# Performance work log

Hardware: AMD Instinct MI355X
Metric: run time of the kernel (lower is better)

## Reference

```python
import jax, jax.numpy as jnp
import numpy as np

B, S, H = 2, 1024, 2048
HQ, HKV, D = 16, 4, 128
E, K, CAP = 32, 4, 512
IM, SIM = 512, 1024
EPS = 1e-6
THETA = 1.0e6
T = B * S


def setup_inputs() -> dict:
    key = jax.random.key(0)
    ks = jax.random.split(key, 16)
    r = lambda i, shape, s=0.02: jax.random.normal(ks[i], shape, dtype=jnp.float32) * s
    return {
        "hidden_states": jax.random.normal(ks[0], (T, H), dtype=jnp.float32),
        "positions": jnp.tile(jnp.arange(S, dtype=jnp.int32), B),
        "ln1_w": jnp.ones((H,), jnp.float32),
        "ln2_w": jnp.ones((H,), jnp.float32),
        "wq": r(1, (H, HQ * D)),
        "wk": r(2, (H, HKV * D)),
        "wv": r(3, (H, HKV * D)),
        "wo": r(4, (HQ * D, H)),
        "qn_w": jnp.ones((D,), jnp.float32),
        "kn_w": jnp.ones((D,), jnp.float32),
        "gate_w": r(5, (H, E), 0.05),
        "expert_bias": r(6, (E,), 0.1),
        "w_gate_e": r(7, (E, H, IM)),
        "w_up_e": r(8, (E, H, IM)),
        "w_down_e": r(9, (E, IM, H)),
        "ws_gate": r(10, (H, SIM)),
        "ws_up": r(11, (H, SIM)),
        "ws_down": r(12, (SIM, H)),
    }


def _rms(x, w):
    return x * jax.lax.rsqrt(jnp.mean(x * x, axis=-1, keepdims=True) + EPS) * w


def _forward(hidden_states, positions, ln1_w, ln2_w, wq, wk, wv, wo, qn_w, kn_w,
             gate_w, expert_bias, w_gate_e, w_up_e, w_down_e, ws_gate, ws_up, ws_down):
    # --- attention block ---
    resid = hidden_states
    h = _rms(hidden_states, ln1_w)
    q = (h @ wq).reshape(T, HQ, D)
    k = (h @ wk).reshape(T, HKV, D)
    v = (h @ wv).reshape(T, HKV, D)
    q = _rms(q, qn_w)  # per-head qk-norm
    k = _rms(k, kn_w)
    # neox-style RoPE over full head_dim
    inv = 1.0 / (THETA ** (jnp.arange(0, D, 2, dtype=jnp.float32) / D))
    fr = positions.astype(jnp.float32)[:, None] * inv  # [T, D/2]
    cos, sin = jnp.cos(fr)[:, None, :], jnp.sin(fr)[:, None, :]
    def rope(x):
        x1, x2 = jnp.split(x, 2, axis=-1)
        return jnp.concatenate([x1 * cos - x2 * sin, x2 * cos + x1 * sin], axis=-1)
    q, k = rope(q), rope(k)
    qb = q.reshape(B, S, HQ, D)
    kb = jnp.repeat(k.reshape(B, S, HKV, D), HQ // HKV, axis=2)  # GQA expand
    vb = jnp.repeat(v.reshape(B, S, HKV, D), HQ // HKV, axis=2)
    sc = jnp.einsum('bqhd,bkhd->bhqk', qb, kb) * (D ** -0.5)
    causal = jnp.tril(jnp.ones((S, S), dtype=bool))
    sc = jnp.where(causal, sc, jnp.float32(-1e30))
    p = jax.nn.softmax(sc, axis=-1)
    ao = jnp.einsum('bhqk,bkhd->bqhd', p, vb).reshape(T, HQ * D)
    h = ao @ wo + resid
    resid = h
    h = _rms(h, ln2_w)
    # --- shared experts (dense MLP) ---
    shared = (jax.nn.silu(h @ ws_gate) * (h @ ws_up)) @ ws_down
    # --- sigmoid router with correction bias (bias only for selection) ---
    scores = jax.nn.sigmoid(h @ gate_w)          # [T, E]
    _, idx = jax.lax.top_k(scores + expert_bias, K)
    w = jnp.take_along_axis(scores, idx, axis=-1)
    w = w / jnp.sum(w, axis=-1, keepdims=True)   # renormalize top-k probs
    # --- capacity-based dispatch / grouped GEMM / combine ---
    flat_e = idx.reshape(-1)                     # [T*K]
    flat_t = jnp.repeat(jnp.arange(T), K)
    flat_w = w.reshape(-1)
    order = jnp.argsort(flat_e)                  # stable sort by expert
    se, st, sw = flat_e[order], flat_t[order], flat_w[order]
    counts = jnp.bincount(flat_e, length=E)
    starts = jnp.concatenate([jnp.zeros((1,), counts.dtype), jnp.cumsum(counts)[:-1]])
    pos = jnp.arange(T * K) - starts[se]         # slot within expert
    valid = pos < CAP                            # capacity guard (never trips in practice)
    posc = jnp.minimum(pos, CAP - 1)
    xbuf = jnp.zeros((E, CAP, H), h.dtype).at[se, posc].add(
        jnp.where(valid[:, None], h[st], 0.0))   # [E, CAP, H]
    inter = jax.nn.silu(jnp.einsum('ech,ehi->eci', xbuf, w_gate_e)) \
            * jnp.einsum('ech,ehi->eci', xbuf, w_up_e)
    obuf = jnp.einsum('eci,eih->ech', inter, w_down_e)
    y = obuf[se, posc] * jnp.where(valid, sw, 0.0)[:, None]
    moe = jnp.zeros((T, H), h.dtype).at[st].add(y)
    return resid + moe + shared


def reference(hidden_states, positions, ln1_w, ln2_w, wq, wk, wv, wo, qn_w, kn_w,
              gate_w, expert_bias, w_gate_e, w_up_e, w_down_e, ws_gate, ws_up, ws_down):
    return _forward(hidden_states, positions, ln1_w, ln2_w, wq, wk, wv, wo, qn_w, kn_w,
                    gate_w, expert_bias, w_gate_e, w_up_e, w_down_e, ws_gate, ws_up, ws_down)
```

## Files before the change

### kernel.cpp

```cpp
#include <hip/hip_runtime.h>
#include <stdint.h>

typedef unsigned short u16;
typedef unsigned short bf16u;
typedef unsigned int u32;
typedef _Float16 f16;
typedef __attribute__((ext_vector_type(8))) short bf16x8;
typedef __attribute__((ext_vector_type(8))) _Float16 f16x8;
typedef __attribute__((ext_vector_type(4))) float f32x4;

#define T_N 2048
#define H_N 2048
#define S_N 1024
#define B_N 2
#define HQ_N 16
#define HKV_N 4
#define D_N 128
#define E_N 32
#define K_TOP 4
#define CAP_N 512
#define IM_N 512
#define SIM_N 1024
#define QD_N 2048
#define KD_N 512
#define QKV_N 3072
#define NFLAT (T_N*K_TOP)
#define RGRP 128
#define NGRP (NFLAT/RGRP)

#define SC_H1   1024.0f
#define SC_W    512.0f
#define SC_QK   2048.0f
#define SC_P    4096.0f
#define SC_V    2048.0f
#define OSC_QKV (1.0f/524288.0f)
#define OSC_OPJ (1.0f/1048576.0f)

__device__ __forceinline__ float bf2f(bf16u x){ return __uint_as_float(((u32)x)<<16); }
__device__ __forceinline__ bf16u f2bf(float f){
  u32 u = __float_as_uint(f);
  u32 r = (u + 0x7FFFu + ((u>>16)&1u)) >> 16;
  return (bf16u)r;
}
__device__ __forceinline__ u32 pkbf(float a, float b){
  u32 ua = __float_as_uint(a), ub = __float_as_uint(b);
  u32 ra = (ua + 0x7FFFu + ((ua>>16)&1u)) >> 16;
  u32 rb = (ub + 0x7FFFu + ((ub>>16)&1u)) & 0xFFFF0000u;
  return ra | rb;
}
__device__ __forceinline__ void split2h(float x, u16& h, u16& l){
  f16 hh = (f16)x;
  f16 ll = (f16)(x - (float)hh);
  h = __builtin_bit_cast(u16, hh);
  l = __builtin_bit_cast(u16, ll);
}
__device__ __forceinline__ f32x4 mfma16b(bf16x8 a, bf16x8 b, f32x4 c){
  return __builtin_amdgcn_mfma_f32_16x16x32_bf16(a,b,c,0,0,0);
}
__device__ __forceinline__ f32x4 mfma16h(f16x8 a, f16x8 b, f32x4 c){
  return __builtin_amdgcn_mfma_f32_16x16x32_f16(a,b,c,0,0,0);
}
__device__ __forceinline__ void gl_lds16(const void* g, void* l){
  __builtin_amdgcn_global_load_lds((const __attribute__((address_space(1))) u32*)g,
                                   (__attribute__((address_space(3))) u32*)l, 16, 0, 0);
}

__global__ __launch_bounds__(256) void transpose_f32(const float* __restrict__ in,
                                                     float* __restrict__ out, int R, int C){
  __shared__ float tile[32][33];
  int rb = blockIdx.x*32, cb = blockIdx.y*32;
  int tx = threadIdx.x, ty = threadIdx.y;
  #pragma unroll
  for (int kk=0;kk<4;kk++)
    tile[ty+kk*8][tx] = in[(size_t)(rb+ty+kk*8)*C + cb + tx];
  __syncthreads();
  #pragma unroll
  for (int kk=0;kk<4;kk++)
    out[(size_t)(cb+ty+kk*8)*R + rb + tx] = tile[tx][ty+kk*8];
}

__global__ __launch_bounds__(256) void transpose_cvt_g(const float* __restrict__ in,
                                                       bf16u* __restrict__ out, int R, int C){
  __shared__ float tile[64*64];
  size_t zo = (size_t)blockIdx.z * R * C;
  int rb = blockIdx.x*64, cb = blockIdx.y*64;
  int tid = threadIdx.x, wave = tid>>6, lane = tid&63;
  #pragma unroll
  for (int p=0;p<4;p++){
    int r = p*16 + wave*4 + (lane>>4);
    const float* src = in + zo + (size_t)(rb + r)*C + cb + (lane&15)*4;
    gl_lds16(src, &tile[(p*16 + wave*4)*64]);
  }
  __syncthreads();
  int c = tid>>2, rq = (tid&3)*16;
  u16 tmp[16];
  #pragma unroll
  for (int j=0;j<16;j++) tmp[j] = f2bf(tile[(rq+j)*64 + c]);
  uint4 w0, w1;
  w0.x=(u32)tmp[0]|((u32)tmp[1]<<16);  w0.y=(u32)tmp[2]|((u32)tmp[3]<<16);
  w0.z=(u32)tmp[4]|((u32)tmp[5]<<16);  w0.w=(u32)tmp[6]|((u32)tmp[7]<<16);
  w1.x=(u32)tmp[8]|((u32)tmp[9]<<16);  w1.y=(u32)tmp[10]|((u32)tmp[11]<<16);
  w1.z=(u32)tmp[12]|((u32)tmp[13]<<16); w1.w=(u32)tmp[14]|((u32)tmp[15]<<16);
  bf16u* dst = out + zo + (size_t)(cb+c)*R + rb + rq;
  *(uint4*)dst = w0;
  *(uint4*)(dst+8) = w1;
}

__global__ __launch_bounds__(256) void transpose_cvt_split16(const float* __restrict__ in,
                                                             u16* __restrict__ oh,
                                                             u16* __restrict__ ol,
                                                             int R, int C, float scale){
  __shared__ u16 th[32][33];
  __shared__ u16 tl[32][33];
  int rb = blockIdx.x*32, cb = blockIdx.y*32;
  int tx = threadIdx.x, ty = threadIdx.y;
  #pragma unroll
  for (int kk=0;kk<4;kk++){
    float x = in[(size_t)(rb+ty+kk*8)*C + cb + tx] * scale;
    u16 hh, ll; split2h(x, hh, ll);
    th[ty+kk*8][tx] = hh; tl[ty+kk*8][tx] = ll;
  }
  __syncthreads();
  #pragma unroll
  for (int kk=0;kk<4;kk++){
    size_t idx = (size_t)(cb+ty+kk*8)*R + rb + tx;
    oh[idx] = th[tx][ty+kk*8];
    ol[idx] = tl[tx][ty+kk*8];
  }
}

__global__ __launch_bounds__(256) void rmsnorm_bf16(const float* __restrict__ x,
                                                    const float* __restrict__ w,
                                                    bf16u* __restrict__ y){
  int row = blockIdx.x; int t = threadIdx.x;
  const float4* x4 = (const float4*)(x + (size_t)row*H_N);
  float4 a = x4[2*t], b = x4[2*t+1];
  float ss = a.x*a.x+a.y*a.y+a.z*a.z+a.w*a.w + b.x*b.x+b.y*b.y+b.z*b.z+b.w*b.w;
  #pragma unroll
  for (int m=32;m>=1;m>>=1) ss += __shfl_xor(ss,m,64);
  __shared__ float red[4];
  if ((t&63)==0) red[t>>6]=ss;
  __syncthreads();
  float scale = rsqrtf((red[0]+red[1]+red[2]+red[3])*(1.0f/H_N) + 1e-6f);
  const float4* w4 = (const float4*)w;
  float4 wa = w4[2*t], wb = w4[2*t+1];
  uint4 pk;
  pk.x = pkbf(a.x*scale*wa.x, a.y*scale*wa.y);
  pk.y = pkbf(a.z*scale*wa.z, a.w*scale*wa.w);
  pk.z = pkbf(b.x*scale*wb.x, b.y*scale*wb.y);
  pk.w = pkbf(b.z*scale*wb.z, b.w*scale*wb.w);
  ((uint4*)(y + (size_t)row*H_N))[t] = pk;
}

__global__ __launch_bounds__(256) void rmsnorm_f16split(const float* __restrict__ x,
                                                        const float* __restrict__ w,
                                                        u16* __restrict__ yh,
                                                        u16* __restrict__ yl){
  int row = blockIdx.x; int t = threadIdx.x;
  const float4* x4 = (const float4*)(x + (size_t)row*H_N);
  float4 a = x4[2*t], b = x4[2*t+1];
  float ss = a.x*a.x+a.y*a.y+a.z*a.z+a.w*a.w + b.x*b.x+b.y*b.y+b.z*b.z+b.w*b.w;
  #pragma unroll
  for (int m=32;m>=1;m>>=1) ss += __shfl_xor(ss,m,64);
  __shared__ float red[4];
  if ((t&63)==0) red[t>>6]=ss;
  __syncthreads();
  float scale = rsqrtf((red[0]+red[1]+red[2]+red[3])*(1.0f/H_N) + 1e-6f) * SC_H1;
  const float4* w4 = (const float4*)w;
  float4 wa = w4[2*t], wb = w4[2*t+1];
  float o[8] = {a.x*scale*wa.x, a.y*scale*wa.y, a.z*scale*wa.z, a.w*scale*wa.w,
                b.x*scale*wb.x, b.y*scale*wb.y, b.z*scale*wb.z, b.w*scale*wb.w};
  u16 hh[8], ll[8];
  #pragma unroll
  for (int j=0;j<8;j++) split2h(o[j], hh[j], ll[j]);
  uint4 pk, pl;
  pk.x = (u32)hh[0]|((u32)hh[1]<<16); pk.y = (u32)hh[2]|((u32)hh[3]<<16);
  pk.z = (u32)hh[4]|((u32)hh[5]<<16); pk.w = (u32)hh[6]|((u32)hh[7]<<16);
  pl.x = (u32)ll[0]|((u32)ll[1]<<16); pl.y = (u32)ll[2]|((u32)ll[3]<<16);
  pl.z = (u32)ll[4]|((u32)ll[5]<<16); pl.w = (u32)ll[6]|((u32)ll[7]<<16);
  ((uint4*)(yh + (size_t)row*H_N))[t] = pk;
  ((uint4*)(yl + (size_t)row*H_N))[t] = pl;
}

__global__ void qknorm_rope_split(const float* __restrict__ qkv,
                                  const float* __restrict__ qw, const float* __restrict__ kw,
                                  const int* __restrict__ positions,
                                  u16* __restrict__ qho, u16* __restrict__ qlo,
                                  u16* __restrict__ kho, u16* __restrict__ klo){
  int t = blockIdx.x; int hy = blockIdx.y; int l = threadIdx.x;
  const float* p; const float* w; u16 *oh, *ol; size_t obase;
  if (hy < HQ_N){
    p = qkv + (size_t)t*QKV_N + hy*D_N; w = qw;
    oh = qho; ol = qlo; obase = (size_t)t*QD_N + hy*D_N;
  } else {
    p = qkv + (size_t)t*QKV_N + QD_N + (hy-HQ_N)*D_N; w = kw;
    oh = kho; ol = klo; obase = (size_t)t*KD_N + (hy-HQ_N)*D_N;
  }
  float x0 = p[l], x1 = p[l+64];
  float ss = x0*x0 + x1*x1;
  #pragma unroll
  for (int m=32;m>=1;m>>=1) ss += __shfl_xor(ss,m,64);
  float scale = rsqrtf(ss*(1.0f/D_N)+1e-6f);
  x0 *= scale*w[l]; x1 *= scale*w[l+64];
  double freq = exp2(-(double)l * (19.931568569324174/64.0));
  double fr = (double)positions[t] * freq;
  double sd, cd; sincos(fr, &sd, &cd);
  float r0 = (float)((double)x0*cd - (double)x1*sd) * SC_QK;
  float r1 = (float)((double)x1*cd + (double)x0*sd) * SC_QK;
  u16 hh, ll;
  split2h(r0, hh, ll); oh[obase+l] = hh; ol[obase+l] = ll;
  split2h(r1, hh, ll); oh[obase+l+64] = hh; ol[obase+l+64] = ll;
}

__global__ __launch_bounds__(256) void transpose_v_split(const float* __restrict__ in,
                                                         u16* __restrict__ oh,
                                                         u16* __restrict__ ol){
  __shared__ u16 th[32][33];
  __shared__ u16 tl[32][33];
  int z = blockIdx.z; int b = z >> 2, kvh = z & 3;
  const float* ip = in + (size_t)b*S_N*QKV_N + QD_N + KD_N + kvh*D_N;
  size_t ob = (size_t)z*D_N*S_N;
  int sb = blockIdx.x*32, db = blockIdx.y*32;
  int tx=threadIdx.x, ty=threadIdx.y;
  #pragma unroll
  for (int kk=0;kk<4;kk++){
    float x = ip[(size_t)(sb+ty+kk*8)*QKV_N + db+tx] * SC_V;
    u16 hh, ll; split2h(x, hh, ll);
    th[ty+kk*8][tx] = hh; tl[ty+kk*8][tx] = ll;
  }
  __syncthreads();
  #pragma unroll
  for (int kk=0;kk<4;kk++){
    size_t idx = ob + (size_t)(db+ty+kk*8)*S_N + sb+tx;
    oh[idx] = th[tx][ty+kk*8];
    ol[idx] = tl[tx][ty+kk*8];
  }
}

template<int MODE, bool SPLIT>
__global__ __launch_bounds__(256) void gemm_bt(
    const u16* __restrict__ A, const u16* __restrict__ Al,
    const u16* __restrict__ B0g, const u16* __restrict__ B0lg,
    const u16* __restrict__ B1g,
    void* __restrict__ Cout, const float* __restrict__ resid, float oscale,
    int N, int Kd)
{
  constexpr bool DUAL = (MODE==2);
  __shared__ u16 As[2][128*32];
  __shared__ u16 Bs0[2][128*32];
  __shared__ u16 Asl[SPLIT?2:1][SPLIT?128*32:8];
  __shared__ u16 Bs0l[SPLIT?2:1][SPLIT?128*32:8];
  __shared__ u16 Bs1[DUAL?2:1][DUAL?128*32:8];

  int tid = threadIdx.x;
  int wave = tid>>6, lane = tid&63, l15 = lane&15, lg = lane>>4;
  int nBase = blockIdx.y*128;
  int mBase = blockIdx.x*128;

  size_t aOff[2], bOff[2];
  #pragma unroll
  for (int i=0;i<2;i++){
    int le = (i*256 + tid)*8;
    int r = le >> 5;
    int c = le & 31;
    aOff[i] = (size_t)(mBase + r)*Kd + c;
    bOff[i] = (size_t)(nBase + r)*Kd + c;
  }

  auto STAGE = [&](int buf, int kt){
    size_t ko = (size_t)kt*32;
    #pragma unroll
    for (int i=0;i<2;i++){
      int lo = i*2048 + wave*512;
      gl_lds16(A + aOff[i] + ko, &As[buf][lo]);
      gl_lds16(B0g + bOff[i] + ko, &Bs0[buf][lo]);
      if constexpr (SPLIT){
        gl_lds16(Al + aOff[i] + ko, &Asl[buf][lo]);
        gl_lds16(B0lg + bOff[i] + ko, &Bs0l[buf][lo]);
      }
      if constexpr (DUAL){
        gl_lds16(B1g + bOff[i] + ko, &Bs1[buf][lo]);
      }
    }
  };

  f32x4 zero4 = {0.f,0.f,0.f,0.f};
  f32x4 acc0[4][4];
  f32x4 acc1[DUAL?4:1][DUAL?4:1];
  #pragma unroll
  for (int mi=0;mi<4;mi++)
    #pragma unroll
    for (int ni=0;ni<4;ni++){
      acc0[mi][ni] = zero4;
      if constexpr (DUAL) acc1[mi][ni] = zero4;
    }

  int wm = wave>>1, wn = wave&1;
  int nK = Kd >> 5;
  STAGE(0, 0);
  __syncthreads();
  for (int kt=0; kt<nK; kt++){
    int cur = kt&1;
    if (kt+1 < nK) STAGE(cur^1, kt+1);
    if constexpr (SPLIT){
      f16x8 af[4], afl[4];
      #pragma unroll
      for (int mi=0;mi<4;mi++){
        af[mi]  = *(const f16x8*)&As [cur][(wm*64 + mi*16 + l15)*32 + lg*8];
        afl[mi] = *(const f16x8*)&Asl[cur][(wm*64 + mi*16 + l15)*32 + lg*8];
      }
      #pragma unroll
      for (int ni=0;ni<4;ni++){
        f16x8 b0  = *(const f16x8*)&Bs0 [cur][(wn*64 + ni*16 + l15)*32 + lg*8];
        f16x8 b0l = *(const f16x8*)&Bs0l[cur][(wn*64 + ni*16 + l15)*32 + lg*8];
        #pragma unroll
        for (int mi=0;mi<4;mi++){
          acc0[mi][ni] = mfma16h(af[mi], b0, acc0[mi][ni]);
          acc0[mi][ni] = mfma16h(af[mi], b0l, acc0[mi][ni]);
          acc0[mi][ni] = mfma16h(afl[mi], b0, acc0[mi][ni]);
        }
      }
    } else {
      bf16x8 af[4];
      #pragma unroll
      for (int mi=0;mi<4;mi++)
        af[mi] = *(const bf16x8*)&As[cur][(wm*64 + mi*16 + l15)*32 + lg*8];
      #pragma unroll
      for (int ni=0;ni<4;ni++){
        bf16x8 b0 = *(const bf16x8*)&Bs0[cur][(wn*64 + ni*16 + l15)*32 + lg*8];
        #pragma unroll
        for (int mi=0;mi<4;mi++) acc0[mi][ni] = mfma16b(af[mi], b0, acc0[mi][ni]);
        if constexpr (DUAL){
          bf16x8 b1 = *(const bf16x8*)&Bs1[cur][(wn*64 + ni*16 + l15)*32 + lg*8];
          #pragma unroll
          for (int mi=0;mi<4;mi++) acc1[mi][ni] = mfma16b(af[mi], b1, acc1[mi][ni]);
        }
      }
    }
    __syncthreads();
  }

  #pragma unroll
  for (int mi=0;mi<4;mi++){
    #pragma unroll
    for (int ni=0;ni<4;ni++){
      #pragma unroll
      for (int i=0;i<4;i++){
        int rloc = wm*64 + mi*16 + 4*lg + i;
        int col  = nBase + wn*64 + ni*16 + l15;
        float v = acc0[mi][ni][i];
        if constexpr (MODE==1){
          size_t idx = (size_t)(mBase + rloc)*N + col;
          ((float*)Cout)[idx] = v*oscale + (resid ? resid[idx] : 0.0f);
        } else {
          float u = acc1[mi][ni][i];
          float sv = v/(1.0f+__expf(-v))*u;
          ((bf16u*)Cout)[(size_t)(mBase + rloc)*N + col] = f2bf(sv);
        }
      }
    }
  }
}

__global__ __launch_bounds__(512) void moe_gu8w(
    const u16* __restrict__ A,
    const u16* __restrict__ B0g,
    const u16* __restrict__ B1g,
    bf16u* __restrict__ Out,
    const int* __restrict__ starts, const int* __restrict__ counts,
    const int* __restrict__ perm)
{
  __shared__ u16 As[2][128*32];
  __shared__ u16 Bs0[2][128*32];
  __shared__ u16 Bs1[2][128*32];

  int e = blockIdx.z;
  int cnt = counts[e]; cnt = cnt < CAP_N ? cnt : CAP_N;
  int mBase = blockIdx.x*128;
  int rows = cnt - mBase;
  if (rows <= 0) return;
  if (rows > 128) rows = 128;
  int slotBase = starts[e] + mBase;
  int nBase = blockIdx.y*128;
  const u16* Bp0 = B0g + (size_t)e*IM_N*H_N;
  const u16* Bp1 = B1g + (size_t)e*IM_N*H_N;

  int tid = threadIdx.x, wave = tid>>6, lane = tid&63, l15 = lane&15, lg = lane>>4;
  int r = tid>>2, c = (tid&3)*8;
  int rr = (r < rows) ? r : 0;
  size_t aOff = (size_t)perm[slotBase + rr]*H_N + c;
  size_t bOff = (size_t)(nBase + r)*H_N + c;

  auto STAGE = [&](int buf, int kt){
    size_t ko = (size_t)kt*32;
    gl_lds16(A + aOff + ko, &As[buf][tid*8]);
    gl_lds16(Bp0 + bOff + ko, &Bs0[buf][tid*8]);
    gl_lds16(Bp1 + bOff + ko, &Bs1[buf][tid*8]);
  };

  f32x4 zero4 = {0.f,0.f,0.f,0.f};
  f32x4 acc0[2][4], acc1[2][4];
  #pragma unroll
  for (int mi=0;mi<2;mi++)
    #pragma unroll
    for (int ni=0;ni<4;ni++){ acc0[mi][ni]=zero4; acc1[mi][ni]=zero4; }

  int wm = wave>>1, wn = wave&1;
  STAGE(0, 0);
  __syncthreads();
  int nK = H_N >> 5;
  for (int kt=0; kt<nK; kt++){
    int cur = kt&1;
    if (kt+1 < nK) STAGE(cur^1, kt+1);
    bf16x8 af[2];
    #pragma unroll
    for (int mi=0;mi<2;mi++)
      af[mi] = *(const bf16x8*)&As[cur][(wm*32 + mi*16 + l15)*32 + lg*8];
    #pragma unroll
    for (int ni=0;ni<4;ni++){
      bf16x8 b0 = *(const bf16x8*)&Bs0[cur][(wn*64 + ni*16 + l15)*32 + lg*8];
      bf16x8 b1 = *(const bf16x8*)&Bs1[cur][(wn*64 + ni*16 + l15)*32 + lg*8];
      #pragma unroll
      for (int mi=0;mi<2;mi++){
        acc0[mi][ni] = mfma16b(af[mi], b0, acc0[mi][ni]);
        acc1[mi][ni] = mfma16b(af[mi], b1, acc1[mi][ni]);
      }
    }
    __syncthreads();
  }

  #pragma unroll
  for (int mi=0;mi<2;mi++){
    #pragma unroll
    for (int ni=0;ni<4;ni++){
      #pragma unroll
      for (int i=0;i<4;i++){
        int rloc = wm*32 + mi*16 + 4*lg + i;
        if (rloc < rows){
          float v = acc0[mi][ni][i];
          float u = acc1[mi][ni][i];
          float sv = v/(1.0f+__expf(-v))*u;
          Out[(size_t)(slotBase + rloc)*IM_N + nBase + wn*64 + ni*16 + l15] = f2bf(sv);
        }
      }
    }
  }
}

__global__ __launch_bounds__(512) void moe_down8w(
    const u16* __restrict__ A,
    const u16* __restrict__ B0g,
    bf16u* __restrict__ Out,
    const int* __restrict__ starts, const int* __restrict__ counts)
{
  __shared__ u16 As[2][128*32];
  __shared__ u16 Bs0[2][128*32];

  int e = blockIdx.z;
  int cnt = counts[e]; cnt = cnt < CAP_N ? cnt : CAP_N;
  int mBase = blockIdx.x*128;
  int rows = cnt - mBase;
  if (rows <= 0) return;
  if (rows > 128) rows = 128;
  int slotBase = starts[e] + mBase;
  int nBase = blockIdx.y*128;
  const u16* Bp0 = B0g + (size_t)e*H_N*IM_N;

  int tid = threadIdx.x, wave = tid>>6, lane = tid&63, l15 = lane&15, lg = lane>>4;
  int r = tid>>2, c = (tid&3)*8;
  int rr = (r < rows) ? r : 0;
  size_t aOff = (size_t)(slotBase + rr)*IM_N + c;
  size_t bOff = (size_t)(nBase + r)*IM_N + c;

  auto STAGE = [&](int buf, int kt){
    size_t ko = (size_t)kt*32;
    gl_lds16(A + aOff + ko, &As[buf][tid*8]);
    gl_lds16(Bp0 + bOff + ko, &Bs0[buf][tid*8]);
  };

  f32x4 zero4 = {0.f,0.f,0.f,0.f};
  f32x4 acc0[2][4];
  #pragma unroll
  for (int mi=0;mi<2;mi++)
    #pragma unroll
    for (int ni=0;ni<4;ni++) acc0[mi][ni]=zero4;

  int wm = wave>>1, wn = wave&1;
  STAGE(0, 0);
  __syncthreads();
  int nK = IM_N >> 5;
  for (int kt=0; kt<nK; kt++){
    int cur = kt&1;
    if (kt+1 < nK) STAGE(cur^1, kt+1);
    bf16x8 af[2];
    #pragma unroll
    for (int mi=0;mi<2;mi++)
      af[mi] = *(const bf16x8*)&As[cur][(wm*32 + mi*16 + l15)*32 + lg*8];
    #pragma unroll
    for (int ni=0;ni<4;ni++){
      bf16x8 b0 = *(const bf16x8*)&Bs0[cur][(wn*64 + ni*16 + l15)*32 + lg*8];
      #pragma unroll
      for (int mi=0;mi<2;mi++)
        acc0[mi][ni] = mfma16b(af[mi], b0, acc0[mi][ni]);
    }
    __syncthreads();
  }

  #pragma unroll
  for (int mi=0;mi<2;mi++){
    #pragma unroll
    for (int ni=0;ni<4;ni++){
      #pragma unroll
      for (int i=0;i<4;i++){
        int rloc = wm*32 + mi*16 + 4*lg + i;
        if (rloc < rows)
          Out[(size_t)(slotBase + rloc)*H_N + nBase + wn*64 + ni*16 + l15] = f2bf(acc0[mi][ni][i]);
      }
    }
  }
}

__global__ __launch_bounds__(256) void attn_kernel(
    const u16* __restrict__ qh, const u16* __restrict__ ql,
    const u16* __restrict__ kh, const u16* __restrict__ kl,
    const u16* __restrict__ vth, const u16* __restrict__ vtl,
    u16* __restrict__ aoh, u16* __restrict__ aol)
{
  int qb = blockIdx.x*64;
  int bh = blockIdx.y;
  int b = bh >> 4, h = bh & 15, kvh = h >> 2;
  int tid = threadIdx.x, wave = tid>>6, lane = tid&63, l15 = lane&15, lg = lane>>4;

  __shared__ u16 Ksh[64*136];
  __shared__ u16 Ksl[64*136];
  __shared__ u16 Vsh[128*72];
  __shared__ u16 Vsl[128*72];
  __shared__ u16 Psh[4][16*72];
  __shared__ u16 Psl[4][16*72];

  size_t qrow = (size_t)(b*S_N + qb + wave*16 + l15)*QD_N + h*D_N;
  f16x8 qfh[4], qfl[4];
  #pragma unroll
  for (int ds=0; ds<4; ds++){
    qfh[ds] = *(const f16x8*)(qh + qrow + ds*32 + lg*8);
    qfl[ds] = *(const f16x8*)(ql + qrow + ds*32 + lg*8);
  }

  f32x4 zero4 = {0.f,0.f,0.f,0.f};
  f32x4 accO[8];
  #pragma unroll
  for (int dc=0; dc<8; dc++) accO[dc] = zero4;
  float mrun[4], lrun[4];
  #pragma unroll
  for (int i=0;i<4;i++){ mrun[i] = -3.0e38f; lrun[i] = 0.0f; }

  const float SC_S = 0.08838834764831845f * (1.0f/(SC_QK*SC_QK));
  int nkt = (qb >> 6) + 1;
  for (int kt=0; kt<nkt; kt++){
    #pragma unroll
    for (int pp=0; pp<4; pp++){
      int r = pp*16 + (tid>>4), c = (tid&15)*8;
      size_t go = (size_t)(b*S_N + kt*64 + r)*KD_N + kvh*D_N + c;
      *(f16x8*)&Ksh[r*136 + c] = *(const f16x8*)(kh + go);
      *(f16x8*)&Ksl[r*136 + c] = *(const f16x8*)(kl + go);
    }
    #pragma unroll
    for (int pp=0; pp<4; pp++){
      int r = pp*32 + (tid>>3), c = (tid&7)*8;
      size_t go = ((size_t)(b*HKV_N + kvh)*D_N + r)*S_N + kt*64 + c;
      *(f16x8*)&Vsh[r*72 + c] = *(const f16x8*)(vth + go);
      *(f16x8*)&Vsl[r*72 + c] = *(const f16x8*)(vtl + go);
    }
    __syncthreads();

    f32x4 sacc[4];
    #pragma unroll
    for (int kc=0;kc<4;kc++){
      sacc[kc] = zero4;
      #pragma unroll
      for (int ds=0; ds<4; ds++){
        f16x8 kfh = *(const f16x8*)&Ksh[(kc*16 + l15)*136 + ds*32 + lg*8];
        f16x8 kfl = *(const f16x8*)&Ksl[(kc*16 + l15)*136 + ds*32 + lg*8];
        sacc[kc] = mfma16h(qfh[ds], kfh, sacc[kc]);
        sacc[kc] = mfma16h(qfh[ds], kfl, sacc[kc]);
        sacc[kc] = mfma16h(qfl[ds], kfh, sacc[kc]);
      }
    }

    float pv[4][4];
    bool last = (kt == nkt-1);
    #pragma unroll
    for (int kc=0;kc<4;kc++)
      #pragma unroll
      for (int i=0;i<4;i++){
        float sv = sacc[kc][i] * SC_S;
        if (last){
          int kg = kt*64 + kc*16 + l15;
          int qg = qb + wave*16 + 4*lg + i;
          if (kg > qg) sv = -3.0e38f;
        }
        pv[kc][i] = sv;
      }

    #pragma unroll
    for (int i=0;i<4;i++){
      float mx = fmaxf(fmaxf(pv[0][i],pv[1][i]),fmaxf(pv[2][i],pv[3][i]));
      #pragma unroll
      for (int mm=1; mm<16; mm<<=1) mx = fmaxf(mx, __shfl_xor(mx, mm, 64));
      float mnew = fmaxf(mrun[i], mx);
      float corr = exp2f((mrun[i]-mnew)*1.44269504f);
      float ps = 0.f;
      #pragma unroll
      for (int kc=0;kc<4;kc++){
        float p = exp2f((pv[kc][i]-mnew)*1.44269504f);
        pv[kc][i] = p; ps += p;
      }
      #pragma unroll
      for (int mm=1; mm<16; mm<<=1) ps += __shfl_xor(ps, mm, 64);
      lrun[i] = lrun[i]*corr + ps;
      mrun[i] = mnew;
      #pragma unroll
      for (int dc=0;dc<8;dc++) accO[dc][i] *= corr;
    }

    #pragma unroll
    for (int kc=0;kc<4;kc++)
      #pragma unroll
      for (int i=0;i<4;i++){
        u16 hh, ll; split2h(pv[kc][i]*SC_P, hh, ll);
        Psh[wave][(4*lg+i)*72 + kc*16 + l15] = hh;
        Psl[wave][(4*lg+i)*72 + kc*16 + l15] = ll;
      }
    asm volatile("s_waitcnt lgkmcnt(0)" ::: "memory");
    __builtin_amdgcn_sched_barrier(0);

    #pragma unroll
    for (int ks=0; ks<2; ks++){
      f16x8 pfh = *(const f16x8*)&Psh[wave][l15*72 + ks*32 + lg*8];
      f16x8 pfl = *(const f16x8*)&Psl[wave][l15*72 + ks*32 + lg*8];
      #pragma unroll
      for (int dc=0; dc<8; dc++){
        f16x8 vfh = *(const f16x8*)&Vsh[(dc*16 + l15)*72 + ks*32 + lg*8];
        f16x8 vfl = *(const f16x8*)&Vsl[(dc*16 + l15)*72 + ks*32 + lg*8];
        accO[dc] = mfma16h(pfh, vfh, accO[dc]);
        accO[dc] = mfma16h(pfh, vfl, accO[dc]);
        accO[dc] = mfma16h(pfl, vfh, accO[dc]);
      }
    }
    __syncthreads();
  }

  #pragma unroll
  for (int i=0;i<4;i++){
    float inv = 1.0f / (4096.0f * lrun[i]);
    size_t orow = (size_t)(b*S_N + qb + wave*16 + 4*lg + i)*QD_N + h*D_N;
    #pragma unroll
    for (int dc=0; dc<8; dc++){
      u16 hh, ll; split2h(accO[dc][i]*inv, hh, ll);
      aoh[orow + dc*16 + l15] = hh;
      aol[orow + dc*16 + l15] = ll;
    }
  }
}

__global__ __launch_bounds__(256) void router_kernel(
    const float* __restrict__ resid2, const float* __restrict__ ln2w,
    const float* __restrict__ gwT, const float* __restrict__ ebias,
    int* __restrict__ tkIdx, float* __restrict__ tkW, int* __restrict__ counts)
{
  int t = blockIdx.x, tid = threadIdx.x;
  __shared__ float xs[H_N];
  __shared__ float red[4];
  __shared__ float sc[E_N];
  const float4* x4 = (const float4*)(resid2 + (size_t)t*H_N);
  float4 a = x4[2*tid], b = x4[2*tid+1];
  float ss = a.x*a.x+a.y*a.y+a.z*a.z+a.w*a.w + b.x*b.x+b.y*b.y+b.z*b.z+b.w*b.w;
  #pragma unroll
  for (int m=32;m>=1;m>>=1) ss += __shfl_xor(ss,m,64);
  if ((tid&63)==0) red[tid>>6]=ss;
  __syncthreads();
  float scale = rsqrtf((red[0]+red[1]+red[2]+red[3])*(1.0f/H_N) + 1e-6f);
  const float4* w4 = (const float4*)ln2w;
  float4 wa = w4[2*tid], wb = w4[2*tid+1];
  xs[tid*8+0]=a.x*scale*wa.x; xs[tid*8+1]=a.y*scale*wa.y;
  xs[tid*8+2]=a.z*scale*wa.z; xs[tid*8+3]=a.w*scale*wa.w;
  xs[tid*8+4]=b.x*scale*wb.x; xs[tid*8+5]=b.y*scale*wb.y;
  xs[tid*8+6]=b.z*scale*wb.z; xs[tid*8+7]=b.w*scale*wb.w;
  __syncthreads();
  int wave = tid>>6, lane = tid&63;
  const float4* xv4 = (const float4*)xs;
  #pragma unroll
  for (int ei=0; ei<8; ei++){
    int e = wave*8 + ei;
    const float4* g4 = (const float4*)(gwT + (size_t)e*H_N);
    float acc = 0.f;
    #pragma unroll
    for (int it=0; it<8; it++){
      int idx = it*64 + lane;
      float4 g = g4[idx], xv = xv4[idx];
      acc += g.x*xv.x + g.y*xv.y + g.z*xv.z + g.w*xv.w;
    }
    #pragma unroll
    for (int m=32;m>=1;m>>=1) acc += __shfl_xor(acc,m,64);
    if (lane==0) sc[e] = 1.0f/(1.0f+__expf(-acc));
  }
  __syncthreads();
  if (tid==0){
    float sb[E_N];
    #pragma unroll
    for (int e2=0;e2<E_N;e2++) sb[e2] = sc[e2]+ebias[e2];
    int ch[4]; float wv[4]; float wsum=0.f;
    for (int j=0;j<4;j++){
      int best=0; float bv=-3.0e38f;
      for (int e2=0;e2<E_N;e2++) if (sb[e2] > bv){ bv=sb[e2]; best=e2; }
      ch[j]=best; wv[j]=sc[best]; wsum+=sc[best]; sb[best]=-3.0e38f;
    }
    float invs = 1.0f/wsum;
    for (int j=0;j<4;j++){
      tkIdx[t*4+j]=ch[j]; tkW[t*4+j]=wv[j]*invs;
      atomicAdd(&counts[ch[j]], 1);
    }
  }
}

__global__ void moe_count_kernel(const int* __restrict__ tki, int* __restrict__ G){
  __shared__ int cnt[E_N];
  int g = blockIdx.x, t = threadIdx.x;
  if (t < E_N) cnt[t] = 0;
  __syncthreads();
  atomicAdd(&cnt[tki[g*RGRP + t]], 1);
  __syncthreads();
  if (t < E_N) G[g*E_N + t] = cnt[t];
}

__global__ void moe_scan_kernel(const int* __restrict__ G, int* __restrict__ base,
                                int* __restrict__ starts){
  __shared__ int tot[E_N];
  int e = threadIdx.x;
  if (e < E_N){
    int run = 0;
    for (int g=0; g<NGRP; g++){ base[g*E_N+e] = run; run += G[g*E_N+e]; }
    tot[e] = run < CAP_N ? run : CAP_N;
  }
  __syncthreads();
  if (e==0){
    int run=0;
    for (int x=0; x<E_N; x++){ starts[x]=run; run+=tot[x]; }
  }
}

__global__ void moe_assign_kernel(const int* __restrict__ tki,
                                  const int* __restrict__ base, const int* __restrict__ starts,
                                  int* __restrict__ ptok, int* __restrict__ tok2slot){
  __shared__ int eL[RGRP];
  int g = blockIdx.x, t = threadIdx.x;
  int f = g*RGRP + t;
  int e = tki[f];
  eL[t] = e;
  __syncthreads();
  int r = 0;
  for (int j=0; j<RGRP; j++) r += ((j < t) && (eL[j]==e)) ? 1 : 0;
  int pos = base[g*E_N + e] + r;
  if (pos < CAP_N){
    int slot = starts[e] + pos;
    ptok[slot] = f >> 2;
    tok2slot[f] = slot;
  } else {
    tok2slot[f] = -1;
  }
}

__global__ __launch_bounds__(256) void moe_combine(const int* __restrict__ tok2slot,
                                                   const float* __restrict__ tkw,
                                                   const bf16u* __restrict__ obuf,
                                                   float* __restrict__ outp){
  int t = blockIdx.x;
  int c0 = threadIdx.x*8;
  float acc[8];
  float4* o4 = (float4*)(outp + (size_t)t*H_N + c0);
  float4 v0 = o4[0], v1 = o4[1];
  acc[0]=v0.x; acc[1]=v0.y; acc[2]=v0.z; acc[3]=v0.w;
  acc[4]=v1.x; acc[5]=v1.y; acc[6]=v1.z; acc[7]=v1.w;
  #pragma unroll
  for (int j=0;j<4;j++){
    int slot = tok2slot[t*4+j];
    if (slot >= 0){
      float w = tkw[t*4+j];
      bf16x8 ob = *(const bf16x8*)(obuf + (size_t)slot*H_N + c0);
      #pragma unroll
      for (int q=0;q<8;q++) acc[q] += w * bf2f((bf16u)ob[q]);
    }
  }
  v0.x=acc[0]; v0.y=acc[1]; v0.z=acc[2]; v0.w=acc[3];
  v1.x=acc[4]; v1.y=acc[5]; v1.z=acc[6]; v1.w=acc[7];
  o4[0]=v0; o4[1]=v1;
}

extern "C" void kernel_launch(void* const* d_in, const int* in_sizes, int n_in,
                              void* d_out, int out_size, void* d_ws, size_t ws_size,
                              hipStream_t stream) {
  (void)in_sizes; (void)n_in; (void)out_size; (void)ws_size;
  const float* hidden    = (const float*)d_in[0];
  const int*   positions = (const int*)d_in[1];
  const float* ln1w = (const float*)d_in[2];
  const float* ln2w = (const float*)d_in[3];
  const float* wq   = (const float*)d_in[4];
  const float* wk   = (const float*)d_in[5];
  const float* wv   = (const float*)d_in[6];
  const float* wo   = (const float*)d_in[7];
  const float* qnw  = (const float*)d_in[8];
  const float* knw  = (const float*)d_in[9];
  const float* gatew= (const float*)d_in[10];
  const float* ebias= (const float*)d_in[11];
  const float* wge  = (const float*)d_in[12];
  const float* wue  = (const float*)d_in[13];
  const float* wde  = (const float*)d_in[14];
  const float* wsg  = (const float*)d_in[15];
  const float* wsu  = (const float*)d_in[16];
  const float* wsd  = (const float*)d_in[17];
  float* outp = (float*)d_out;

  char* wsb = (char*)d_ws;
  size_t off = 0;
  auto take = [&](size_t bytes)->char*{
    char* p = wsb + off; off += (bytes + 255) & ~(size_t)255; return p;
  };
  u16* qkvTh = (u16*)take(3072ull*2048*2);
  u16* qkvTl = (u16*)take(3072ull*2048*2);
  u16* woTh = (u16*)take(2048ull*2048*2);
  u16* woTl = (u16*)take(2048ull*2048*2);
  u16* wsgT = (u16*)take(1024ull*2048*2);
  u16* wsuT = (u16*)take(1024ull*2048*2);
  u16* wsdT = (u16*)take(2048ull*1024*2);
  u16* wgeT = (u16*)take(32ull*512*2048*2);
  u16* wueT = (u16*)take(32ull*512*2048*2);
  u16* wdeT = (u16*)take(32ull*2048*512*2);
  float* gwT = (float*)take(32ull*2048*4);
  u16* h1h  = (u16*)take((size_t)T_N*H_N*2);
  u16* h1l  = (u16*)take((size_t)T_N*H_N*2);
  float* qkv32 = (float*)take((size_t)T_N*QKV_N*4);
  u16* qHh  = (u16*)take((size_t)T_N*QD_N*2);
  u16* qHl  = (u16*)take((size_t)T_N*QD_N*2);
  u16* kHh  = (u16*)take((size_t)T_N*KD_N*2);
  u16* kHl  = (u16*)take((size_t)T_N*KD_N*2);
  u16* vtHh = (u16*)take((size_t)T_N*KD_N*2);
  u16* vtHl = (u16*)take((size_t)T_N*KD_N*2);
  u16* aoh  = (u16*)take((size_t)T_N*QD_N*2);
  u16* aol  = (u16*)take((size_t)T_N*QD_N*2);
  float* resid2=(float*)take((size_t)T_N*H_N*4);
  u16* h2   = (u16*)take((size_t)T_N*H_N*2);
  u16* interS=(u16*)take((size_t)T_N*SIM_N*2);
  u16* minter=(u16*)take((size_t)NFLAT*IM_N*2);
  bf16u* obuf = (bf16u*)take((size_t)NFLAT*H_N*2);
  int*   tki  = (int*)take((size_t)NFLAT*4);
  float* tkw  = (float*)take((size_t)NFLAT*4);
  int*   counts=(int*)take(E_N*4);
  int*   Gcnt = (int*)take((size_t)NGRP*E_N*4);
  int*   Gbase= (int*)take((size_t)NGRP*E_N*4);
  int*   starts=(int*)take(E_N*4);
  int*   ptok = (int*)take((size_t)NFLAT*4);
  int*   tok2slot = (int*)take((size_t)NFLAT*4);

  hipMemsetAsync(counts, 0, 256, stream);

  dim3 tb(32,8);
  transpose_cvt_split16<<<dim3(64,64,1), tb, 0, stream>>>(wq, qkvTh, qkvTl, 2048, 2048, SC_W);
  transpose_cvt_split16<<<dim3(64,16,1), tb, 0, stream>>>(wk, qkvTh + 2048ull*2048, qkvTl + 2048ull*2048, 2048, 512, SC_W);
  transpose_cvt_split16<<<dim3(64,16,1), tb, 0, stream>>>(wv, qkvTh + 2560ull*2048, qkvTl + 2560ull*2048, 2048, 512, SC_W);
  transpose_cvt_split16<<<dim3(64,64,1), tb, 0, stream>>>(wo, woTh, woTl, 2048, 2048, SC_W);
  transpose_cvt_g<<<dim3(32,16,1), 256, 0, stream>>>(wsg, wsgT, 2048, 1024);
  transpose_cvt_g<<<dim3(32,16,1), 256, 0, stream>>>(wsu, wsuT, 2048, 1024);
  transpose_cvt_g<<<dim3(16,32,1), 256, 0, stream>>>(wsd, wsdT, 1024, 2048);
  transpose_cvt_g<<<dim3(32,8,32), 256, 0, stream>>>(wge, wgeT, 2048, 512);
  transpose_cvt_g<<<dim3(32,8,32), 256, 0, stream>>>(wue, wueT, 2048, 512);
  transpose_cvt_g<<<dim3(8,32,32), 256, 0, stream>>>(wde, wdeT, 512, 2048);
  transpose_f32<<<dim3(64,1,1), tb, 0, stream>>>(gatew, gwT, 2048, 32);

  rmsnorm_f16split<<<T_N, 256, 0, stream>>>(hidden, ln1w, h1h, h1l);
  gemm_bt<1,true><<<dim3(16,24), 256, 0, stream>>>(h1h, h1l, qkvTh, qkvTl, nullptr, qkv32, nullptr, OSC_QKV, QKV_N, H_N);
  qknorm_rope_split<<<dim3(T_N,20), 64, 0, stream>>>(qkv32, qnw, knw, positions, qHh, qHl, kHh, kHl);
  transpose_v_split<<<dim3(32,4,8), tb, 0, stream>>>(qkv32, vtHh, vtHl);
  attn_kernel<<<dim3(16,32), 256, 0, stream>>>(qHh, qHl, kHh, kHl, vtHh, vtHl, aoh, aol);
  gemm_bt<1,true><<<dim3(16,16), 256, 0, stream>>>(aoh, aol, woTh, woTl, nullptr, resid2, hidden, OSC_OPJ, H_N, QD_N);
  rmsnorm_bf16<<<T_N, 256, 0, stream>>>(resid2, ln2w, (bf16u*)h2);
  gemm_bt<2,false><<<dim3(16,8), 256, 0, stream>>>(h2, nullptr, wsgT, nullptr, wsuT, interS, nullptr, 1.0f, SIM_N, H_N);
  gemm_bt<1,false><<<dim3(16,16), 256, 0, stream>>>(interS, nullptr, wsdT, nullptr, nullptr, outp, resid2, 1.0f, H_N, SIM_N);
  router_kernel<<<T_N, 256, 0, stream>>>(resid2, ln2w, gwT, ebias, tki, tkw, counts);
  moe_count_kernel<<<NGRP, RGRP, 0, stream>>>(tki, Gcnt);
  moe_scan_kernel<<<1, 64, 0, stream>>>(Gcnt, Gbase, starts);
  moe_assign_kernel<<<NGRP, RGRP, 0, stream>>>(tki, Gbase, starts, ptok, tok2slot);
  moe_gu8w<<<dim3(4,4,32), 512, 0, stream>>>(h2, wgeT, wueT, minter, starts, counts, ptok);
  moe_down8w<<<dim3(4,16,32), 512, 0, stream>>>(minter, wdeT, obuf, starts, counts);
  moe_combine<<<T_N, 256, 0, stream>>>(tok2slot, tkw, obuf, outp);
}
```

Measured before the change: 884.3 us.

## Pair causal query tiles per attention block and vectorize split-weight transposes

The attention kernel now runs 512 threads per block. Each block pairs query tile bx with tile 15-bx, so every block does a balanced amount of causal work, and the loaded K/V tiles are shared by both query tiles. Waves whose tile is already past the diagonal skip compute but still join the barriers. The fp16 hi/lo weight transpose is also rewritten to use 64x64 LDS tiles with direct global-to-LDS loads and 16-byte stores, cutting preprocessing overhead. The main risk is that idle waves in half the block lower utilization near the end of each block's loop.

```diff
diff --git a/kernel.cpp b/kernel.cpp
--- a/kernel.cpp
+++ b/kernel.cpp
@@ -106,27 +106,36 @@
   *(uint4*)(dst+8) = w1;
 }
 
-__global__ __launch_bounds__(256) void transpose_cvt_split16(const float* __restrict__ in,
-                                                             u16* __restrict__ oh,
-                                                             u16* __restrict__ ol,
-                                                             int R, int C, float scale){
-  __shared__ u16 th[32][33];
-  __shared__ u16 tl[32][33];
-  int rb = blockIdx.x*32, cb = blockIdx.y*32;
-  int tx = threadIdx.x, ty = threadIdx.y;
-  #pragma unroll
-  for (int kk=0;kk<4;kk++){
-    float x = in[(size_t)(rb+ty+kk*8)*C + cb + tx] * scale;
-    u16 hh, ll; split2h(x, hh, ll);
-    th[ty+kk*8][tx] = hh; tl[ty+kk*8][tx] = ll;
-  }
-  __syncthreads();
-  #pragma unroll
-  for (int kk=0;kk<4;kk++){
-    size_t idx = (size_t)(cb+ty+kk*8)*R + rb + tx;
-    oh[idx] = th[tx][ty+kk*8];
-    ol[idx] = tl[tx][ty+kk*8];
-  }
+__global__ __launch_bounds__(256) void transpose_split16_g(const float* __restrict__ in,
+                                                           u16* __restrict__ oh,
+                                                           u16* __restrict__ ol,
+                                                           int R, int C, float scale){
+  __shared__ float tile[64*64];
+  int rb = blockIdx.x*64, cb = blockIdx.y*64;
+  int tid = threadIdx.x, wave = tid>>6, lane = tid&63;
+  #pragma unroll
+  for (int p=0;p<4;p++){
+    int r = p*16 + wave*4 + (lane>>4);
+    const float* src = in + (size_t)(rb + r)*C + cb + (lane&15)*4;
+    gl_lds16(src, &tile[(p*16 + wave*4)*64]);
+  }
+  __syncthreads();
+  int c = tid>>2, rq = (tid&3)*16;
+  u16 th[16], tl[16];
+  #pragma unroll
+  for (int j=0;j<16;j++) split2h(tile[(rq+j)*64 + c]*scale, th[j], tl[j]);
+  uint4 h0, h1, l0, l1;
+  h0.x=(u32)th[0]|((u32)th[1]<<16);  h0.y=(u32)th[2]|((u32)th[3]<<16);
+  h0.z=(u32)th[4]|((u32)th[5]<<16);  h0.w=(u32)th[6]|((u32)th[7]<<16);
+  h1.x=(u32)th[8]|((u32)th[9]<<16);  h1.y=(u32)th[10]|((u32)th[11]<<16);
+  h1.z=(u32)th[12]|((u32)th[13]<<16); h1.w=(u32)th[14]|((u32)th[15]<<16);
+  l0.x=(u32)tl[0]|((u32)tl[1]<<16);  l0.y=(u32)tl[2]|((u32)tl[3]<<16);
+  l0.z=(u32)tl[4]|((u32)tl[5]<<16);  l0.w=(u32)tl[6]|((u32)tl[7]<<16);
+  l1.x=(u32)tl[8]|((u32)tl[9]<<16);  l1.y=(u32)tl[10]|((u32)tl[11]<<16);
+  l1.z=(u32)tl[12]|((u32)tl[13]<<16); l1.w=(u32)tl[14]|((u32)tl[15]<<16);
+  size_t o = (size_t)(cb+c)*R + rb + rq;
+  *(uint4*)(oh + o) = h0; *(uint4*)(oh + o + 8) = h1;
+  *(uint4*)(ol + o) = l0; *(uint4*)(ol + o + 8) = l1;
 }
 
 __global__ __launch_bounds__(256) void rmsnorm_bf16(const float* __restrict__ x,
@@ -520,13 +529,13 @@
   }
 }
 
-__global__ __launch_bounds__(256) void attn_kernel(
+__global__ __launch_bounds__(512) void attn_kernel(
     const u16* __restrict__ qh, const u16* __restrict__ ql,
     const u16* __restrict__ kh, const u16* __restrict__ kl,
     const u16* __restrict__ vth, const u16* __restrict__ vtl,
     u16* __restrict__ aoh, u16* __restrict__ aol)
 {
-  int qb = blockIdx.x*64;
+  int bx = blockIdx.x;
   int bh = blockIdx.y;
   int b = bh >> 4, h = bh & 15, kvh = h >> 2;
   int tid = threadIdx.x, wave = tid>>6, lane = tid&63, l15 = lane&15, lg = lane>>4;
@@ -535,10 +544,14 @@
   __shared__ u16 Ksl[64*136];
   __shared__ u16 Vsh[128*72];
   __shared__ u16 Vsl[128*72];
-  __shared__ u16 Psh[4][16*72];
-  __shared__ u16 Psl[4][16*72];
-
-  size_t qrow = (size_t)(b*S_N + qb + wave*16 + l15)*QD_N + h*D_N;
+  __shared__ u16 Psh[8][16*72];
+  __shared__ u16 Psl[8][16*72];
+
+  int qtile = (wave < 4) ? bx : (15 - bx);
+  int wl = wave & 3;
+  int qrow0 = qtile*64 + wl*16;
+
+  size_t qrow = (size_t)(b*S_N + qrow0 + l15)*QD_N + h*D_N;
   f16x8 qfh[4], qfl[4];
   #pragma unroll
   for (int ds=0; ds<4; ds++){
@@ -555,96 +568,99 @@
   for (int i=0;i<4;i++){ mrun[i] = -3.0e38f; lrun[i] = 0.0f; }
 
   const float SC_S = 0.08838834764831845f * (1.0f/(SC_QK*SC_QK));
-  int nkt = (qb >> 6) + 1;
+  int nkt = 16 - bx;
   for (int kt=0; kt<nkt; kt++){
     #pragma unroll
-    for (int pp=0; pp<4; pp++){
-      int r = pp*16 + (tid>>4), c = (tid&15)*8;
+    for (int pp=0; pp<2; pp++){
+      int r = pp*32 + (tid>>4), c = (tid&15)*8;
       size_t go = (size_t)(b*S_N + kt*64 + r)*KD_N + kvh*D_N + c;
       *(f16x8*)&Ksh[r*136 + c] = *(const f16x8*)(kh + go);
       *(f16x8*)&Ksl[r*136 + c] = *(const f16x8*)(kl + go);
     }
     #pragma unroll
-    for (int pp=0; pp<4; pp++){
-      int r = pp*32 + (tid>>3), c = (tid&7)*8;
+    for (int pp=0; pp<2; pp++){
+      int r = pp*64 + (tid>>3), c = (tid&7)*8;
       size_t go = ((size_t)(b*HKV_N + kvh)*D_N + r)*S_N + kt*64 + c;
       *(f16x8*)&Vsh[r*72 + c] = *(const f16x8*)(vth + go);
       *(f16x8*)&Vsl[r*72 + c] = *(const f16x8*)(vtl + go);
     }
     __syncthreads();
 
-    f32x4 sacc[4];
-    #pragma unroll
-    for (int kc=0;kc<4;kc++){
-      sacc[kc] = zero4;
-      #pragma unroll
-      for (int ds=0; ds<4; ds++){
-        f16x8 kfh = *(const f16x8*)&Ksh[(kc*16 + l15)*136 + ds*32 + lg*8];
-        f16x8 kfl = *(const f16x8*)&Ksl[(kc*16 + l15)*136 + ds*32 + lg*8];
-        sacc[kc] = mfma16h(qfh[ds], kfh, sacc[kc]);
-        sacc[kc] = mfma16h(qfh[ds], kfl, sacc[kc]);
-        sacc[kc] = mfma16h(qfl[ds], kfh, sacc[kc]);
-      }
-    }
-
-    float pv[4][4];
-    bool last = (kt == nkt-1);
-    #pragma unroll
-    for (int kc=0;kc<4;kc++)
+    bool active = (kt <= qtile);
+    if (active){
+      f32x4 sacc[4];
+      #pragma unroll
+      for (int kc=0;kc<4;kc++){
+        sacc[kc] = zero4;
+        #pragma unroll
+        for (int ds=0; ds<4; ds++){
+          f16x8 kfh = *(const f16x8*)&Ksh[(kc*16 + l15)*136 + ds*32 + lg*8];
+          f16x8 kfl = *(const f16x8*)&Ksl[(kc*16 + l15)*136 + ds*32 + lg*8];
+          sacc[kc] = mfma16h(qfh[ds], kfh, sacc[kc]);
+          sacc[kc] = mfma16h(qfh[ds], kfl, sacc[kc]);
+          sacc[kc] = mfma16h(qfl[ds], kfh, sacc[kc]);
+        }
+      }
+
+      float pv[4][4];
+      bool maskT = (kt == qtile);
+      #pragma unroll
+      for (int kc=0;kc<4;kc++)
+        #pragma unroll
+        for (int i=0;i<4;i++){
+          float sv = sacc[kc][i] * SC_S;
+          if (maskT){
+            int kg = kt*64 + kc*16 + l15;
+            int qg = qrow0 + 4*lg + i;
+            if (kg > qg) sv = -3.0e38f;
+          }
+          pv[kc][i] = sv;
+        }
+
       #pragma unroll
       for (int i=0;i<4;i++){
-        float sv = sacc[kc][i] * SC_S;
-        if (last){
-          int kg = kt*64 + kc*16 + l15;
-          int qg = qb + wave*16 + 4*lg + i;
-          if (kg > qg) sv = -3.0e38f;
+        float mx = fmaxf(fmaxf(pv[0][i],pv[1][i]),fmaxf(pv[2][i],pv[3][i]));
+        #pragma unroll
+        for (int mm=1; mm<16; mm<<=1) mx = fmaxf(mx, __shfl_xor(mx, mm, 64));
+        float mnew = fmaxf(mrun[i], mx);
+        float corr = exp2f((mrun[i]-mnew)*1.44269504f);
+        float ps = 0.f;
+        #pragma unroll
+        for (int kc=0;kc<4;kc++){
+          float p = exp2f((pv[kc][i]-mnew)*1.44269504f);
+          pv[kc][i] = p; ps += p;
         }
-        pv[kc][i] = sv;
-      }
-
-    #pragma unroll
-    for (int i=0;i<4;i++){
-      float mx = fmaxf(fmaxf(pv[0][i],pv[1][i]),fmaxf(pv[2][i],pv[3][i]));
-      #pragma unroll
-      for (int mm=1; mm<16; mm<<=1) mx = fmaxf(mx, __shfl_xor(mx, mm, 64));
-      float mnew = fmaxf(mrun[i], mx);
-      float corr = exp2f((mrun[i]-mnew)*1.44269504f);
-      float ps = 0.f;
-      #pragma unroll
-      for (int kc=0;kc<4;kc++){
-        float p = exp2f((pv[kc][i]-mnew)*1.44269504f);
-        pv[kc][i] = p; ps += p;
-      }
-      #pragma unroll
-      for (int mm=1; mm<16; mm<<=1) ps += __shfl_xor(ps, mm, 64);
-      lrun[i] = lrun[i]*corr + ps;
-      mrun[i] = mnew;
-      #pragma unroll
-      for (int dc=0;dc<8;dc++) accO[dc][i] *= corr;
-    }
-
-    #pragma unroll
-    for (int kc=0;kc<4;kc++)
-      #pragma unroll
-      for (int i=0;i<4;i++){
-        u16 hh, ll; split2h(pv[kc][i]*SC_P, hh, ll);
-        Psh[wave][(4*lg+i)*72 + kc*16 + l15] = hh;
-        Psl[wave][(4*lg+i)*72 + kc*16 + l15] = ll;
-      }
-    asm volatile("s_waitcnt lgkmcnt(0)" ::: "memory");
-    __builtin_amdgcn_sched_barrier(0);
-
-    #pragma unroll
-    for (int ks=0; ks<2; ks++){
-      f16x8 pfh = *(const f16x8*)&Psh[wave][l15*72 + ks*32 + lg*8];
-      f16x8 pfl = *(const f16x8*)&Psl[wave][l15*72 + ks*32 + lg*8];
-      #pragma unroll
-      for (int dc=0; dc<8; dc++){
-        f16x8 vfh = *(const f16x8*)&Vsh[(dc*16 + l15)*72 + ks*32 + lg*8];
-        f16x8 vfl = *(const f16x8*)&Vsl[(dc*16 + l15)*72 + ks*32 + lg*8];
-        accO[dc] = mfma16h(pfh, vfh, accO[dc]);
-        accO[dc] = mfma16h(pfh, vfl, accO[dc]);
-        accO[dc] = mfma16h(pfl, vfh, accO[dc]);
+        #pragma unroll
+        for (int mm=1; mm<16; mm<<=1) ps += __shfl_xor(ps, mm, 64);
+        lrun[i] = lrun[i]*corr + ps;
+        mrun[i] = mnew;
+        #pragma unroll
+        for (int dc=0;dc<8;dc++) accO[dc][i] *= corr;
+      }
+
+      #pragma unroll
+      for (int kc=0;kc<4;kc++)
+        #pragma unroll
+        for (int i=0;i<4;i++){
+          u16 hh, ll; split2h(pv[kc][i]*SC_P, hh, ll);
+          Psh[wave][(4*lg+i)*72 + kc*16 + l15] = hh;
+          Psl[wave][(4*lg+i)*72 + kc*16 + l15] = ll;
+        }
+      asm volatile("s_waitcnt lgkmcnt(0)" ::: "memory");
+      __builtin_amdgcn_sched_barrier(0);
+
+      #pragma unroll
+      for (int ks=0; ks<2; ks++){
+        f16x8 pfh = *(const f16x8*)&Psh[wave][l15*72 + ks*32 + lg*8];
+        f16x8 pfl = *(const f16x8*)&Psl[wave][l15*72 + ks*32 + lg*8];
+        #pragma unroll
+        for (int dc=0; dc<8; dc++){
+          f16x8 vfh = *(const f16x8*)&Vsh[(dc*16 + l15)*72 + ks*32 + lg*8];
+          f16x8 vfl = *(const f16x8*)&Vsl[(dc*16 + l15)*72 + ks*32 + lg*8];
+          accO[dc] = mfma16h(pfh, vfh, accO[dc]);
+          accO[dc] = mfma16h(pfh, vfl, accO[dc]);
+          accO[dc] = mfma16h(pfl, vfh, accO[dc]);
+        }
       }
     }
     __syncthreads();
@@ -653,7 +669,7 @@
   #pragma unroll
   for (int i=0;i<4;i++){
     float inv = 1.0f / (4096.0f * lrun[i]);
-    size_t orow = (size_t)(b*S_N + qb + wave*16 + 4*lg + i)*QD_N + h*D_N;
+    size_t orow = (size_t)(b*S_N + qrow0 + 4*lg + i)*QD_N + h*D_N;
     #pragma unroll
     for (int dc=0; dc<8; dc++){
       u16 hh, ll; split2h(accO[dc][i]*inv, hh, ll);
@@ -864,10 +880,10 @@
   hipMemsetAsync(counts, 0, 256, stream);
 
   dim3 tb(32,8);
-  transpose_cvt_split16<<<dim3(64,64,1), tb, 0, stream>>>(wq, qkvTh, qkvTl, 2048, 2048, SC_W);
-  transpose_cvt_split16<<<dim3(64,16,1), tb, 0, stream>>>(wk, qkvTh + 2048ull*2048, qkvTl + 2048ull*2048, 2048, 512, SC_W);
-  transpose_cvt_split16<<<dim3(64,16,1), tb, 0, stream>>>(wv, qkvTh + 2560ull*2048, qkvTl + 2560ull*2048, 2048, 512, SC_W);
-  transpose_cvt_split16<<<dim3(64,64,1), tb, 0, stream>>>(wo, woTh, woTl, 2048, 2048, SC_W);
+  transpose_split16_g<<<dim3(32,32), 256, 0, stream>>>(wq, qkvTh, qkvTl, 2048, 2048, SC_W);
+  transpose_split16_g<<<dim3(32,8),  256, 0, stream>>>(wk, qkvTh + 2048ull*2048, qkvTl + 2048ull*2048, 2048, 512, SC_W);
+  transpose_split16_g<<<dim3(32,8),  256, 0, stream>>>(wv, qkvTh + 2560ull*2048, qkvTl + 2560ull*2048, 2048, 512, SC_W);
+  transpose_split16_g<<<dim3(32,32), 256, 0, stream>>>(wo, woTh, woTl, 2048, 2048, SC_W);
   transpose_cvt_g<<<dim3(32,16,1), 256, 0, stream>>>(wsg, wsgT, 2048, 1024);
   transpose_cvt_g<<<dim3(32,16,1), 256, 0, stream>>>(wsu, wsuT, 2048, 1024);
   transpose_cvt_g<<<dim3(16,32,1), 256, 0, stream>>>(wsd, wsdT, 1024, 2048);
@@ -880,7 +896,7 @@
   gemm_bt<1,true><<<dim3(16,24), 256, 0, stream>>>(h1h, h1l, qkvTh, qkvTl, nullptr, qkv32, nullptr, OSC_QKV, QKV_N, H_N);
   qknorm_rope_split<<<dim3(T_N,20), 64, 0, stream>>>(qkv32, qnw, knw, positions, qHh, qHl, kHh, kHl);
   transpose_v_split<<<dim3(32,4,8), tb, 0, stream>>>(qkv32, vtHh, vtHl);
-  attn_kernel<<<dim3(16,32), 256, 0, stream>>>(qHh, qHl, kHh, kHl, vtHh, vtHl, aoh, aol);
+  attn_kernel<<<dim3(8,32), 512, 0, stream>>>(qHh, qHl, kHh, kHl, vtHh, vtHl, aoh, aol);
   gemm_bt<1,true><<<dim3(16,16), 256, 0, stream>>>(aoh, aol, woTh, woTl, nullptr, resid2, hidden, OSC_OPJ, H_N, QD_N);
   rmsnorm_bf16<<<T_N, 256, 0, stream>>>(resid2, ln2w, (bf16u*)h2);
   gemm_bt<2,false><<<dim3(16,8), 256, 0, stream>>>(h2, nullptr, wsgT, nullptr, wsuT, interS, nullptr, 1.0f, SIM_N, H_N);
```

Result: faster. 829.9 us (-6.2%).
